# Kernel tuning notes

Measured on AMD Instinct MI355X. Metric: run time of the kernel, lower is better.

## Reference

```python
import jax, jax.numpy as jnp
import numpy as np

B, S, C, H = 2, 4096, 640, 8
D = C // H  # head_dim = 80


def setup_inputs() -> dict:
    key = jax.random.key(0)
    ks = jax.random.split(key, 5)
    init = 0.02
    return {
        "hidden_states": jax.random.normal(ks[0], (B, S, C), dtype=jnp.float32),
        "Wq": jax.random.normal(ks[1], (C, C), dtype=jnp.float32) * init,
        "Wk": jax.random.normal(ks[2], (C, C), dtype=jnp.float32) * init,
        "Wv": jax.random.normal(ks[3], (C, C), dtype=jnp.float32) * init,
        "Wo": jax.random.normal(ks[4], (C, C), dtype=jnp.float32) * init,
        "bo": jnp.zeros((C,), dtype=jnp.float32),
    }


def reference(hidden_states, Wq, Wk, Wv, Wo, bo):
    # self-attention: encoder_hidden_states is None -> k,v from hidden_states
    x = hidden_states  # [B, S, C]
    q = jnp.einsum("bsc,cd->bsd", x, Wq)
    k = jnp.einsum("bsc,cd->bsd", x, Wk)
    v = jnp.einsum("bsc,cd->bsd", x, Wv)

    # head_to_batch_dim: [B, S, H*D] -> [B, H, S, D]
    def split_heads(t):
        return t.reshape(B, S, H, D).transpose(0, 2, 1, 3)

    q, k, v = split_heads(q), split_heads(k), split_heads(v)

    scale = 1.0 / jnp.sqrt(jnp.float32(D))
    # get_attention_scores: baddbmm(q, k^T) * scale, softmax over keys
    scores = jnp.einsum("bhqd,bhkd->bhqk", q, k) * scale  # [B, H, S, S]
    probs = jax.nn.softmax(scores, axis=-1)
    out = jnp.einsum("bhqk,bhkd->bhqd", probs, v)  # [B, H, S, D]

    # batch_to_head_dim + to_out[0] linear (Dropout is identity at eval)
    out = out.transpose(0, 2, 1, 3).reshape(B, S, C)
    out = jnp.einsum("bsc,cd->bsd", out, Wo) + bo
    # residual_connection=False, rescale_output_factor=1.0 (diffusers defaults)
    return out
```

## Files before the change

kernel.cpp:

```cpp
#include <hip/hip_runtime.h>
#include <hip/hip_bf16.h>

typedef __bf16 bf16x8 __attribute__((ext_vector_type(8)));
typedef float f32x4 __attribute__((ext_vector_type(4)));
typedef float f32x16 __attribute__((ext_vector_type(16)));
typedef unsigned short u16;
typedef unsigned int u32;
typedef u16 u16x8 __attribute__((ext_vector_type(8)));

#define DEV __device__ __forceinline__

DEV u16 f2b(float f) {
    u32 u = __builtin_bit_cast(u32, f);
    u32 r = (u + 0x7FFFu + ((u >> 16) & 1u)) >> 16;
    return (u16)r;
}
DEV bf16x8 load8(const u16* p) {
    return __builtin_bit_cast(bf16x8, *(const uint4*)p);
}
DEV u32 cvtpk(float lo, float hi) {
    u32 r;
    asm("v_cvt_pk_bf16_f32 %0, %1, %2" : "=v"(r) : "v"(lo), "v"(hi));
    return r;
}
DEV void gld_lds16(const u16* g, const char* l) {
    __builtin_amdgcn_global_load_lds(
        (const __attribute__((address_space(1))) u32*)(unsigned long long)g,
        (__attribute__((address_space(3))) u32*)(u32)(unsigned long long)l,
        16, 0, 0);
}

__global__ __launch_bounds__(256) void cvt_all(
    const float* __restrict__ X, u16* __restrict__ Xb,
    const float* __restrict__ Wq, const float* __restrict__ Wk,
    const float* __restrict__ Wv, const float* __restrict__ Wo,
    u16* __restrict__ Wt4)
{
    const int bx = blockIdx.x;
    if (bx < 2560) {
        long i = ((long)bx * 256 + threadIdx.x) * 8;
        float fa[8];
        *(uint4*)fa = *(const uint4*)(X + i);
        *(uint4*)(fa + 4) = *(const uint4*)(X + i + 4);
        u16x8 t;
        #pragma unroll
        for (int j = 0; j < 8; ++j) t[j] = f2b(fa[j]);
        *(u16x8*)(Xb + i) = t;
        return;
    }
    const int idx = bx - 2560;
    const int z = idx / 100;
    const int rem = idx % 100;
    const int k0 = (rem / 10) * 64, n0 = (rem % 10) * 64;
    const float* W = (z == 0) ? Wq : ((z == 1) ? Wk : ((z == 2) ? Wv : Wo));
    u16* Wt = Wt4 + (long)z * 409600;
    const int t = threadIdx.x;
    __shared__ u16 T[64][72];
    {
        int kl = t >> 2, nc = (t & 3) * 16;
        const float* src = W + (long)(k0 + kl) * 640 + n0 + nc;
        float fa[16];
        #pragma unroll
        for (int i = 0; i < 4; ++i) *(uint4*)(fa + i * 4) = *(const uint4*)(src + i * 4);
        #pragma unroll
        for (int j = 0; j < 16; ++j) T[nc + j][kl] = f2b(fa[j]);
    }
    __syncthreads();
    {
        int nl = t >> 2, kc = (t & 3) * 16;
        u16* dst = Wt + (long)(n0 + nl) * 640 + k0 + kc;
        *(uint4*)dst = *(const uint4*)&T[nl][kc];
        *(uint4*)(dst + 8) = *(const uint4*)&T[nl][kc + 8];
    }
}

#define GEMM_CORE(A_PTR, BT_PTR)                                                  \
    const int tid = threadIdx.x;                                                  \
    const int lane = tid & 63;                                                    \
    const int w = tid >> 6;                                                       \
    const int wm = w >> 1, wn = w & 1;                                            \
    const int lg = lane >> 4, lr = lane & 15;                                     \
    __shared__ __align__(16) char Bb[2][16384];                                   \
    auto stage = [&](int kt0, int buf) {                                          \
        _Pragma("unroll")                                                         \
        for (int i = 0; i < 4; ++i) {                                             \
            int c = i * 256 + tid;                                                \
            int n = c >> 3, cc = c & 7;                                           \
            gld_lds16(BT_PTR + (long)(n0 + n) * 640 + kt0 + ((cc ^ (n & 7)) * 8), \
                      Bb[buf] + (c & ~63) * 16);                                  \
        }                                                                         \
    };                                                                            \
    f32x4 acc[4][4] = {};                                                         \
    stage(0, 0);                                                                  \
    for (int t = 0; t < 10; ++t) {                                                \
        __syncthreads();                                                          \
        if (t < 9) stage((t + 1) * 64, (t + 1) & 1);                              \
        const char* Bc = Bb[t & 1];                                               \
        _Pragma("unroll")                                                         \
        for (int ks = 0; ks < 64; ks += 32) {                                     \
            bf16x8 a[4], b[4];                                                    \
            _Pragma("unroll")                                                     \
            for (int mi = 0; mi < 4; ++mi) {                                      \
                int row = m0 + wm * 64 + mi * 16 + lr;                            \
                a[mi] = load8(A_PTR + (long)row * 640 + t * 64 + ks + lg * 8);    \
            }                                                                     \
            _Pragma("unroll")                                                     \
            for (int ni = 0; ni < 4; ++ni) {                                      \
                int n = wn * 64 + ni * 16 + lr;                                   \
                int cc = (ks >> 3) + lg;                                          \
                b[ni] = __builtin_bit_cast(bf16x8,                                \
                    *(const uint4*)(Bc + (n * 8 + (cc ^ (n & 7))) * 16));         \
            }                                                                     \
            _Pragma("unroll")                                                     \
            for (int mi = 0; mi < 4; ++mi)                                        \
                _Pragma("unroll")                                                 \
                for (int ni = 0; ni < 4; ++ni)                                    \
                    acc[mi][ni] = __builtin_amdgcn_mfma_f32_16x16x32_bf16(        \
                        a[mi], b[ni], acc[mi][ni], 0, 0, 0);                      \
        }                                                                         \
    }

__global__ __launch_bounds__(256, 3) void gemm_qkv(
    const u16* __restrict__ X, const u16* __restrict__ Wt3,
    u16* __restrict__ q_ws, u16* __restrict__ k_ws, u16* __restrict__ v_ws)
{
    const int z = blockIdx.z;
    const u16* Wt = Wt3 + (long)z * 409600;
    const int m0 = blockIdx.x * 128;
    const int n0 = blockIdx.y * 128;
    GEMM_CORE(X, Wt)
    #pragma unroll
    for (int mi = 0; mi < 4; ++mi)
        #pragma unroll
        for (int ni = 0; ni < 4; ++ni) {
            const int mbase = m0 + wm * 64 + mi * 16 + lg * 4;
            const int n = n0 + wn * 64 + ni * 16 + lr;
            const int h = n / 80, d = n % 80;
            if (z == 2) {
                int b_ = mbase >> 12, s0 = mbase & 4095;
                long bh = b_ * 8 + h;
                int tt = s0 >> 6, jj0 = s0 & 63;
                int kb = jj0 >> 5, h2 = (jj0 >> 4) & 1, hv = (jj0 >> 2) & 1;
                int jv0 = ((jj0 >> 3) & 1) * 4;
                int c = kb * 2 + h2;
                u16* vt = v_ws + (bh * 64 + tt) * 6144;
                uint2 pk;
                pk.x = cvtpk(acc[mi][ni][0], acc[mi][ni][1]);
                pk.y = cvtpk(acc[mi][ni][2], acc[mi][ni][3]);
                *(uint2*)(vt + ((c * 2 + hv) * 96 + d) * 8 + jv0) = pk;
                if (d == 0) {
                    uint2 ones; ones.x = 0x3F803F80u; ones.y = 0x3F803F80u;
                    *(uint2*)(vt + ((c * 2 + hv) * 96 + 80) * 8 + jv0) = ones;
                }
            } else {
                #pragma unroll
                for (int r = 0; r < 4; ++r) {
                    int m = mbase + r;
                    int b_ = m >> 12, s = m & 4095;
                    long bh = b_ * 8 + h;
                    int tt = s >> 6, jj = s & 63;
                    float val = acc[mi][ni][r];
                    if (z == 0) {
                        q_ws[(bh * 4096 + s) * 80 + d] = f2b(val * 0.16131517891624225f);
                    } else {
                        k_ws[(bh * 64 + tt) * 5120 + (((d >> 4) * 2 + ((d >> 3) & 1)) * 64 + jj) * 8 + (d & 7)] = f2b(val);
                    }
                }
            }
        }
}

__global__ __launch_bounds__(256, 3) void gemm_out(
    const u16* __restrict__ X, const u16* __restrict__ Wt,
    const float* __restrict__ bias, float* __restrict__ out)
{
    const int m0 = blockIdx.x * 128;
    const int n0 = blockIdx.y * 128;
    GEMM_CORE(X, Wt)
    #pragma unroll
    for (int mi = 0; mi < 4; ++mi)
        #pragma unroll
        for (int ni = 0; ni < 4; ++ni)
            #pragma unroll
            for (int r = 0; r < 4; ++r) {
                int m = m0 + wm * 64 + mi * 16 + lg * 4 + r;
                int n = n0 + wn * 64 + ni * 16 + lr;
                out[(long)m * 640 + n] = acc[mi][ni][r] + bias[n];
            }
}

__global__ __launch_bounds__(256, 2) void attn(
    const u16* __restrict__ q_ws, const u16* __restrict__ k_ws,
    const u16* __restrict__ v_ws, u16* __restrict__ o_ws)
{
    const int l = blockIdx.x;
    const int xcd = l & 7, inner = l >> 3;
    const int bh = (xcd << 1) | (inner >> 5);
    const int qx = inner & 31;
    const int qb = qx * 128;
    const int tid = threadIdx.x;
    const int lane = tid & 63;
    const int w = tid >> 6;
    const int hi = lane >> 5;
    const int lq = lane & 31;

    __shared__ __align__(16) char Kb[2][10240];
    __shared__ __align__(16) char Vb[3][12288];

    const u16* ktile = k_ws + (long)bh * 64 * 5120;
    const u16* vtile = v_ws + (long)bh * 64 * 6144;

    bf16x8 qf[5];
    const int qrow = qb + w * 32 + lq;
    #pragma unroll
    for (int kc = 0; kc < 5; ++kc)
        qf[kc] = load8(q_ws + ((long)bh * 4096 + qrow) * 80 + kc * 16 + hi * 8);

    f32x16 acc[3] = {};

    auto stageK = [&](int t, int buf) {
        const u16* kt_ = ktile + (long)t * 5120;
        #pragma unroll
        for (int i = 0; i < 3; ++i) {
            int c = i * 256 + tid;
            if (c < 640) gld_lds16(kt_ + (long)c * 8, Kb[buf] + (c & ~63) * 16);
        }
    };
    auto stageV = [&](int t, int buf) {
        const u16* vt_ = vtile + (long)t * 6144;
        #pragma unroll
        for (int i = 0; i < 3; ++i) {
            int c = i * 256 + tid;
            gld_lds16(vt_ + (long)c * 8, Vb[buf] + (c & ~63) * 16);
        }
    };
    auto QK = [&](int kbuf, f32x16* sf) {
        const char* Kc = Kb[kbuf];
        f32x16 z = {};
        sf[0] = z; sf[1] = z;
        __builtin_amdgcn_s_setprio(1);
        #pragma unroll
        for (int kc = 0; kc < 5; ++kc) {
            #pragma unroll
            for (int kb = 0; kb < 2; ++kb) {
                bf16x8 kf = __builtin_bit_cast(bf16x8,
                    *(const uint4*)(Kc + ((kc * 2 + hi) * 64 + kb * 32 + lq) * 16));
                sf[kb] = __builtin_amdgcn_mfma_f32_32x32x16_bf16(kf, qf[kc], sf[kb], 0, 0, 0);
            }
        }
        __builtin_amdgcn_s_setprio(0);
    };
    auto SM_PV = [&](f32x16* sf, int vbuf) {
        const char* Vc = Vb[vbuf];
        #pragma unroll
        for (int kb = 0; kb < 2; ++kb)
            #pragma unroll
            for (int r = 0; r < 16; ++r)
                sf[kb][r] = __builtin_amdgcn_exp2f(sf[kb][r]);
        bf16x8 pa[4];
        #pragma unroll
        for (int kb = 0; kb < 2; ++kb)
            #pragma unroll
            for (int h = 0; h < 2; ++h) {
                uint4 wv;
                wv.x = cvtpk(sf[kb][h * 8 + 0], sf[kb][h * 8 + 1]);
                wv.y = cvtpk(sf[kb][h * 8 + 2], sf[kb][h * 8 + 3]);
                wv.z = cvtpk(sf[kb][h * 8 + 4], sf[kb][h * 8 + 5]);
                wv.w = cvtpk(sf[kb][h * 8 + 6], sf[kb][h * 8 + 7]);
                pa[kb * 2 + h] = __builtin_bit_cast(bf16x8, wv);
            }
        __builtin_amdgcn_s_setprio(1);
        #pragma unroll
        for (int db = 0; db < 3; ++db)
            #pragma unroll
            for (int c = 0; c < 4; ++c) {
                bf16x8 vf = __builtin_bit_cast(bf16x8,
                    *(const uint4*)(Vc + ((c * 2 + hi) * 96 + db * 32 + lq) * 16));
                acc[db] = __builtin_amdgcn_mfma_f32_32x32x16_bf16(pa[c], vf, acc[db], 0, 0, 0);
            }
        __builtin_amdgcn_s_setprio(0);
    };

    f32x16 sfA[2], sfB[2];
    stageK(0, 0); stageV(0, 0);
    __syncthreads();
    stageK(1, 1); stageV(1, 1);
    QK(0, sfA);

    for (int t = 0; t < 64; t += 2) {
        __syncthreads();
        {
            int ts = (t + 2 < 64) ? t + 2 : 63;
            stageK(ts, t & 1);
            stageV(ts, (t + 2) % 3);
        }
        QK((t + 1) & 1, sfB);
        SM_PV(sfA, t % 3);
        __syncthreads();
        {
            int ts = (t + 3 < 64) ? t + 3 : 63;
            stageK(ts, (t + 1) & 1);
            stageV(ts, (t + 3) % 3);
        }
        QK(t & 1, sfA);
        SM_PV(sfB, (t + 1) % 3);
    }

    const int b_ = bh >> 3, h8 = bh & 7;
    #pragma unroll
    for (int r = 0; r < 16; ++r) {
        int ql = (r & 3) + 8 * (r >> 2) + 4 * hi;
        float lsum = __shfl(acc[2][r], (hi << 5) + 16);
        float inv = 1.0f / lsum;
        int row = qb + w * 32 + ql;
        #pragma unroll
        for (int db = 0; db < 3; ++db) {
            int d = db * 32 + lq;
            if (d < 80)
                o_ws[((long)b_ * 4096 + row) * 640 + h8 * 80 + d] = f2b(acc[db][r] * inv);
        }
    }
}

extern "C" void kernel_launch(void* const* d_in, const int* in_sizes, int n_in,
                              void* d_out, int out_size, void* d_ws, size_t ws_size,
                              hipStream_t stream) {
    const float* x  = (const float*)d_in[0];
    const float* Wq = (const float*)d_in[1];
    const float* Wk = (const float*)d_in[2];
    const float* Wv = (const float*)d_in[3];
    const float* Wo = (const float*)d_in[4];
    const float* bo = (const float*)d_in[5];

    u16* ws = (u16*)d_ws;
    const long SZ = 5242880;
    u16* Xb   = ws;
    u16* q_ws = ws + SZ;
    u16* k_ws = ws + 2 * SZ;
    u16* v_ws = ws + 3 * SZ;
    u16* Wt4  = ws + 3 * SZ + 6291456;
    u16* o_ws = Xb;
    u16* WtO  = Wt4 + 3 * 409600;

    cvt_all<<<2960, 256, 0, stream>>>(x, Xb, Wq, Wk, Wv, Wo, Wt4);

    dim3 g1(64, 5, 3);
    gemm_qkv<<<g1, 256, 0, stream>>>(Xb, Wt4, q_ws, k_ws, v_ws);

    attn<<<512, 256, 0, stream>>>(q_ws, k_ws, v_ws, o_ws);

    dim3 g3(64, 5);
    gemm_out<<<g3, 256, 0, stream>>>(o_ws, WtO, bo, (float*)d_out);
}
```

Measured before the change: 189.6 us.

## Load K tiles directly from global into registers instead of LDS

```diff
diff --git a/kernel.cpp b/kernel.cpp
--- a/kernel.cpp
+++ b/kernel.cpp
@@ -204,7 +204,6 @@
     const int hi = lane >> 5;
     const int lq = lane & 31;
 
-    __shared__ __align__(16) char Kb[2][10240];
     __shared__ __align__(16) char Vb[3][12288];
 
     const u16* ktile = k_ws + (long)bh * 64 * 5120;
@@ -218,14 +217,6 @@
 
     f32x16 acc[3] = {};
 
-    auto stageK = [&](int t, int buf) {
-        const u16* kt_ = ktile + (long)t * 5120;
-        #pragma unroll
-        for (int i = 0; i < 3; ++i) {
-            int c = i * 256 + tid;
-            if (c < 640) gld_lds16(kt_ + (long)c * 8, Kb[buf] + (c & ~63) * 16);
-        }
-    };
     auto stageV = [&](int t, int buf) {
         const u16* vt_ = vtile + (long)t * 6144;
         #pragma unroll
@@ -234,20 +225,23 @@
             gld_lds16(vt_ + (long)c * 8, Vb[buf] + (c & ~63) * 16);
         }
     };
-    auto QK = [&](int kbuf, f32x16* sf) {
-        const char* Kc = Kb[kbuf];
+    auto loadK = [&](int t, bf16x8* kr) {
+        const u16* kt_ = ktile + (long)t * 5120;
+        #pragma unroll
+        for (int kc = 0; kc < 5; ++kc)
+            #pragma unroll
+            for (int kb = 0; kb < 2; ++kb)
+                kr[kc * 2 + kb] = load8(kt_ + ((kc * 2 + hi) * 64 + kb * 32 + lq) * 8);
+    };
+    auto QK = [&](const bf16x8* kr, f32x16* sf) {
         f32x16 z = {};
         sf[0] = z; sf[1] = z;
         __builtin_amdgcn_s_setprio(1);
         #pragma unroll
-        for (int kc = 0; kc < 5; ++kc) {
-            #pragma unroll
-            for (int kb = 0; kb < 2; ++kb) {
-                bf16x8 kf = __builtin_bit_cast(bf16x8,
-                    *(const uint4*)(Kc + ((kc * 2 + hi) * 64 + kb * 32 + lq) * 16));
-                sf[kb] = __builtin_amdgcn_mfma_f32_32x32x16_bf16(kf, qf[kc], sf[kb], 0, 0, 0);
-            }
-        }
+        for (int kc = 0; kc < 5; ++kc)
+            #pragma unroll
+            for (int kb = 0; kb < 2; ++kb)
+                sf[kb] = __builtin_amdgcn_mfma_f32_32x32x16_bf16(kr[kc * 2 + kb], qf[kc], sf[kb], 0, 0, 0);
         __builtin_amdgcn_s_setprio(0);
     };
     auto SM_PV = [&](f32x16* sf, int vbuf) {
@@ -282,27 +276,30 @@
     };
 
     f32x16 sfA[2], sfB[2];
-    stageK(0, 0); stageV(0, 0);
+    bf16x8 krA[10], krB[10];
+    loadK(0, krA);
+    stageV(0, 0);
     __syncthreads();
-    stageK(1, 1); stageV(1, 1);
-    QK(0, sfA);
+    stageV(1, 1);
+    loadK(1, krB);
+    QK(krA, sfA);
 
     for (int t = 0; t < 64; t += 2) {
         __syncthreads();
         {
             int ts = (t + 2 < 64) ? t + 2 : 63;
-            stageK(ts, t & 1);
             stageV(ts, (t + 2) % 3);
-        }
-        QK((t + 1) & 1, sfB);
+            loadK(ts, krA);
+        }
+        QK(krB, sfB);
         SM_PV(sfA, t % 3);
         __syncthreads();
         {
             int ts = (t + 3 < 64) ? t + 3 : 63;
-            stageK(ts, (t + 1) & 1);
             stageV(ts, (t + 3) % 3);
-        }
-        QK(t & 1, sfA);
+            loadK(ts, krB);
+        }
+        QK(krA, sfA);
         SM_PV(sfB, (t + 1) % 3);
     }
 
```

Measured after the change: 195.4 us. 3.1% more time.
